# Performance work log

Hardware: AMD Instinct MI355X
Metric: run time of the kernel (lower is better)

The kernel has to match this reference:

```python
import math
import jax, jax.numpy as jnp
import numpy as np

NUM_HEADS = 8
TOP_M = 5
CLAMP_LOGIT = 2.0
LN_EPS = 1e-5


def _layernorm(x, w, b):
    m = jnp.mean(x, axis=-1, keepdims=True)
    v = jnp.mean((x - m) ** 2, axis=-1, keepdims=True)
    return (x - m) * jax.lax.rsqrt(v + LN_EPS) * w + b


def _l2norm(x, eps=1e-6):
    n = jnp.sqrt(jnp.sum(x * x, axis=-1, keepdims=True))
    return x / jnp.maximum(n, eps)


def setup_inputs() -> dict:
    key = jax.random.key(0)
    ks = jax.random.split(key, 20)
    B, H, W, Cv = 8, 64, 64, 512
    T, Ct = 77, 512
    s = 0.02
    inp = {
        'visual_features': jax.random.normal(ks[0], (B, H, W, Cv), jnp.float32),
        'text_features': jax.random.normal(ks[1], (B, T, Ct), jnp.float32),
        'norm1_w': jnp.ones((Cv,), jnp.float32),
        'norm1_b': jnp.zeros((Cv,), jnp.float32),
        'Wq': jax.random.normal(ks[2], (Cv, Cv), jnp.float32) * s,
        'bq': jnp.zeros((Cv,), jnp.float32),
        'Wk': jax.random.normal(ks[3], (Ct, Cv), jnp.float32) * s,
        'bk': jnp.zeros((Cv,), jnp.float32),
        'Wv': jax.random.normal(ks[4], (Ct, Cv), jnp.float32) * s,
        'bv': jnp.zeros((Cv,), jnp.float32),
        'Wo': jax.random.normal(ks[5], (Cv, Cv), jnp.float32) * s,
        'bo': jnp.zeros((Cv,), jnp.float32),
        'gate_w': jax.random.normal(ks[6], (Cv, 1), jnp.float32) * s,
        'gate_b': jnp.zeros((1,), jnp.float32),
        'norm2_w': jnp.ones((Cv,), jnp.float32),
        'norm2_b': jnp.zeros((Cv,), jnp.float32),
        'ffn_w1': jax.random.normal(ks[7], (Cv, 4 * Cv), jnp.float32) * s,
        'ffn_b1': jnp.zeros((4 * Cv,), jnp.float32),
        'ffn_w2': jax.random.normal(ks[8], (4 * Cv, Cv), jnp.float32) * s,
        'ffn_b2': jnp.zeros((Cv,), jnp.float32),
        'logit_scale': jnp.asarray(math.log(1.0 / 0.07), jnp.float32),
        'alpha': jnp.asarray(0.1, jnp.float32),
    }
    return inp


def reference(visual_features, text_features, norm1_w, norm1_b, Wq, bq, Wk, bk,
              Wv, bv, Wo, bo, gate_w, gate_b, norm2_w, norm2_b,
              ffn_w1, ffn_b1, ffn_w2, ffn_b2, logit_scale, alpha):
    B, H, W, Cv = visual_features.shape
    N = H * W
    Hh = NUM_HEADS
    Dh = Cv // Hh

    # Pre-LN + projections
    x = _layernorm(visual_features, norm1_w, norm1_b).reshape(B, N, Cv)
    q_full = x @ Wq + bq                       # (B,N,Cv)
    k_full = text_features @ Wk + bk           # (B,T,Cv)
    v_full = text_features @ Wv + bv           # (B,T,Cv)

    # pad mask: all-zero text tokens (B,T)
    pad_mask = jnp.sum(jnp.abs(text_features), axis=-1) <= 1e-6

    # cosine attention: normalize over full Cv before splitting heads (as in source)
    q = _l2norm(q_full).reshape(B, N, Hh, Dh)
    k = _l2norm(k_full).reshape(B, -1, Hh, Dh)
    v = v_full.reshape(B, -1, Hh, Dh)

    scale = jnp.exp(jnp.clip(logit_scale, -CLAMP_LOGIT, CLAMP_LOGIT)) / math.sqrt(Dh)
    sim = jnp.einsum('bnhd,bthd->bnht', q, k) * scale  # (B,N,Hh,T)
    sim = jnp.where(pad_mask[:, None, None, :], -jnp.inf, sim)

    # top-k sparsification along text dim (keep entries >= k-th largest)
    if TOP_M < sim.shape[-1]:
        topv = jax.lax.top_k(sim, TOP_M)[0]
        kth = topv[..., -1:]
        sim = jnp.where(sim >= kth, sim, -jnp.inf)

    attn = jax.nn.softmax(sim, axis=-1)
    aligned = jnp.einsum('bnht,bthd->bnhd', attn, v).reshape(B, N, Cv)
    aligned = aligned @ Wo + bo

    gate = jax.nn.sigmoid(x @ gate_w + gate_b)  # (B,N,1)
    y = x + alpha * gate * aligned
    y = _layernorm(y, norm2_w, norm2_b)
    h = jax.nn.gelu(y @ ffn_w1 + ffn_b1, approximate=False)
    y = y + (h @ ffn_w2 + ffn_b2)
    return y.reshape(B, H, W, Cv)
```

## Files before the change

### kernel.cpp

```cpp
#include <hip/hip_runtime.h>
#include <hip/hip_bf16.h>
#include <math.h>

constexpr int Bv = 8;
constexpr int Nv = 4096;
constexpr int Cvd = 512;
constexpr int Tt = 77;
constexpr int Dh = 64;
constexpr int MROWS = Bv * Nv;
constexpr int KTROWS = Bv * Tt;

typedef __attribute__((ext_vector_type(8))) short bf16x8;
typedef __attribute__((ext_vector_type(4))) float f32x4;

__device__ __forceinline__ float bfbits2f(short s) {
    unsigned int u = ((unsigned int)(unsigned short)s) << 16;
    return __uint_as_float(u);
}

__device__ __forceinline__ void gload16(const void* g, void* l) {
    __builtin_amdgcn_global_load_lds(
        (const __attribute__((address_space(1))) void*)g,
        (__attribute__((address_space(3))) void*)l, 16, 0, 0);
}

__device__ __forceinline__ void block_barrier() {
    asm volatile("" ::: "memory");
    __builtin_amdgcn_s_barrier();
    asm volatile("" ::: "memory");
}

__global__ __launch_bounds__(256)
void wtrans4_kernel(const float* __restrict__ Wq, const float* __restrict__ Wo,
                    const float* __restrict__ w1, const float* __restrict__ w2,
                    __hip_bfloat16* __restrict__ WqT, __hip_bfloat16* __restrict__ WoT,
                    __hip_bfloat16* __restrict__ w1T, __hip_bfloat16* __restrict__ w2T)
{
    __shared__ float tile[32][33];
    const int bid = blockIdx.x;
    const float* in;
    __hip_bfloat16* out;
    int K, N, tid;
    if (bid < 256)       { in = Wq; out = WqT; K = 512;  N = 512;  tid = bid; }
    else if (bid < 512)  { in = Wo; out = WoT; K = 512;  N = 512;  tid = bid - 256; }
    else if (bid < 1536) { in = w1; out = w1T; K = 512;  N = 2048; tid = bid - 512; }
    else                 { in = w2; out = w2T; K = 2048; N = 512;  tid = bid - 1536; }
    const int nx = N >> 5;
    const int n0 = (tid % nx) * 32, k0 = (tid / nx) * 32;
    const int tx = threadIdx.x & 31, ty = threadIdx.x >> 5;
    #pragma unroll
    for (int i = ty; i < 32; i += 8)
        tile[i][tx] = in[(size_t)(k0 + i) * N + n0 + tx];
    __syncthreads();
    #pragma unroll
    for (int i = ty; i < 32; i += 8)
        out[(size_t)(n0 + i) * K + k0 + tx] = __float2bfloat16(tile[tx][i]);
}

template<bool GATE>
__global__ __launch_bounds__(128)
void ln_kernel(const float* __restrict__ in, const float* __restrict__ w,
               const float* __restrict__ b, float* __restrict__ out,
               __hip_bfloat16* __restrict__ out_bf,
               const float* __restrict__ gate_w, const float* __restrict__ gate_b,
               float* __restrict__ gate_out)
{
    __shared__ float red[4];
    __shared__ float redg[2];
    const int row = blockIdx.x;
    const int t = threadIdx.x;
    const int wv = t >> 6;
    const float4 v = ((const float4*)(in + (size_t)row * Cvd))[t];

    float s  = v.x + v.y + v.z + v.w;
    float ss = v.x*v.x + v.y*v.y + v.z*v.z + v.w*v.w;
    #pragma unroll
    for (int o = 1; o < 64; o <<= 1) {
        s  += __shfl_xor(s,  o);
        ss += __shfl_xor(ss, o);
    }
    if ((t & 63) == 0) { red[wv*2] = s; red[wv*2+1] = ss; }
    __syncthreads();
    s  = red[0] + red[2];
    ss = red[1] + red[3];
    const float m   = s * (1.0f / 512.0f);
    const float var = ss * (1.0f / 512.0f) - m * m;
    const float rs  = 1.0f / sqrtf(var + 1e-5f);

    const float4 w4 = ((const float4*)w)[t];
    const float4 b4 = ((const float4*)b)[t];
    float4 o4;
    o4.x = (v.x - m) * rs * w4.x + b4.x;
    o4.y = (v.y - m) * rs * w4.y + b4.y;
    o4.z = (v.z - m) * rs * w4.z + b4.z;
    o4.w = (v.w - m) * rs * w4.w + b4.w;
    ((float4*)(out + (size_t)row * Cvd))[t] = o4;

    __hip_bfloat162 h0, h1;
    h0.x = __float2bfloat16(o4.x); h0.y = __float2bfloat16(o4.y);
    h1.x = __float2bfloat16(o4.z); h1.y = __float2bfloat16(o4.w);
    __hip_bfloat16* obp = out_bf + (size_t)row * Cvd + 4*t;
    *(__hip_bfloat162*)(obp)     = h0;
    *(__hip_bfloat162*)(obp + 2) = h1;

    if (GATE) {
        const float4 g4 = ((const float4*)gate_w)[t];
        float g = o4.x*g4.x + o4.y*g4.y + o4.z*g4.z + o4.w*g4.w;
        #pragma unroll
        for (int o = 1; o < 64; o <<= 1) g += __shfl_xor(g, o);
        if ((t & 63) == 0) redg[wv] = g;
        __syncthreads();
        if (t == 0) {
            const float gt = redg[0] + redg[1] + gate_b[0];
            gate_out[row] = 1.0f / (1.0f + expf(-gt));
        }
    }
}

__global__ __launch_bounds__(64)
void rownorm_bf_kernel(const __hip_bfloat16* __restrict__ src, float* __restrict__ inv)
{
    const int row = blockIdx.x;
    const int l = threadIdx.x;
    const bf16x8 v = ((const bf16x8*)(src + (size_t)row * Cvd))[l];
    float ss = 0.0f;
    #pragma unroll
    for (int j = 0; j < 8; j++) {
        const float f = bfbits2f(v[j]);
        ss += f * f;
    }
    #pragma unroll
    for (int o = 1; o < 64; o <<= 1) ss += __shfl_xor(ss, o);
    if (l == 0) inv[row] = 1.0f / fmaxf(sqrtf(ss), 1e-6f);
}

__global__ __launch_bounds__(64)
void knorm_mask_kernel(const float* __restrict__ kf, const float* __restrict__ text,
                       float* __restrict__ kinv, float* __restrict__ msk)
{
    const int row = blockIdx.x;
    const int l = threadIdx.x;
    const float4* rp = (const float4*)(kf + (size_t)row * Cvd);
    const float4* tp = (const float4*)(text + (size_t)row * Cvd);
    const float4 a = rp[l], c = rp[l + 64];
    const float4 ta = tp[l], tc = tp[l + 64];
    float ss = a.x*a.x + a.y*a.y + a.z*a.z + a.w*a.w
             + c.x*c.x + c.y*c.y + c.z*c.z + c.w*c.w;
    float sa = fabsf(ta.x)+fabsf(ta.y)+fabsf(ta.z)+fabsf(ta.w)
             + fabsf(tc.x)+fabsf(tc.y)+fabsf(tc.z)+fabsf(tc.w);
    #pragma unroll
    for (int o = 1; o < 64; o <<= 1) {
        ss += __shfl_xor(ss, o);
        sa += __shfl_xor(sa, o);
    }
    if (l == 0) {
        kinv[row] = 1.0f / fmaxf(sqrtf(ss), 1e-6f);
        msk[row]  = (sa <= 1e-6f) ? 1.0f : 0.0f;
    }
}

__global__ __launch_bounds__(256)
void gemm32kv_kernel(const float* __restrict__ A,
                     const float* __restrict__ Wk, const float* __restrict__ bk,
                     float* __restrict__ Ck,
                     const float* __restrict__ Wv, const float* __restrict__ bv,
                     float* __restrict__ Cv2,
                     int M, int K)
{
    __shared__ float As[16][64 + 4];
    __shared__ float Bs[16][64 + 4];

    const float* W    = blockIdx.z ? Wv  : Wk;
    const float* bias = blockIdx.z ? bv  : bk;
    float*       C    = blockIdx.z ? Cv2 : Ck;

    const int t = threadIdx.x;
    const int tx = t & 15, ty = t >> 4;
    const int row0 = blockIdx.y * 64;
    const int col0 = blockIdx.x * 64;

    const int arow = t >> 2;
    const int ak   = (t & 3) << 2;
    const int brow = t >> 4;
    const int bcol = (t & 15) << 2;

    float acc[4][4] = {};

    for (int kt = 0; kt < K; kt += 16) {
        float4 a4 = make_float4(0.f, 0.f, 0.f, 0.f);
        const int gr = row0 + arow;
        if (gr < M) a4 = *(const float4*)(A + (size_t)gr * 512 + kt + ak);
        As[ak + 0][arow] = a4.x;
        As[ak + 1][arow] = a4.y;
        As[ak + 2][arow] = a4.z;
        As[ak + 3][arow] = a4.w;
        const float4 b4 = *(const float4*)(W + (size_t)(kt + brow) * 512 + col0 + bcol);
        *(float4*)&Bs[brow][bcol] = b4;
        __syncthreads();
        #pragma unroll
        for (int k = 0; k < 16; k++) {
            const float4 av = *(const float4*)&As[k][ty << 2];
            const float4 bv4 = *(const float4*)&Bs[k][tx << 2];
            acc[0][0] += av.x * bv4.x; acc[0][1] += av.x * bv4.y;
            acc[0][2] += av.x * bv4.z; acc[0][3] += av.x * bv4.w;
            acc[1][0] += av.y * bv4.x; acc[1][1] += av.y * bv4.y;
            acc[1][2] += av.y * bv4.z; acc[1][3] += av.y * bv4.w;
            acc[2][0] += av.z * bv4.x; acc[2][1] += av.z * bv4.y;
            acc[2][2] += av.z * bv4.z; acc[2][3] += av.z * bv4.w;
            acc[3][0] += av.w * bv4.x; acc[3][1] += av.w * bv4.y;
            acc[3][2] += av.w * bv4.z; acc[3][3] += av.w * bv4.w;
        }
        __syncthreads();
    }

    #pragma unroll
    for (int i = 0; i < 4; i++) {
        const int r = row0 + (ty << 2) + i;
        if (r >= M) continue;
        #pragma unroll
        for (int j = 0; j < 4; j++) {
            const int c = col0 + (tx << 2) + j;
            C[(size_t)r * 512 + c] = acc[i][j] + bias[c];
        }
    }
}

enum { EPI_NONE = 0, EPI_WO = 1, EPI_GELU = 2, EPI_RES = 3, EPI_QBF = 4 };

template<int NT, int EPI>
__global__ __launch_bounds__(256, 3)
void bgemm_kernel(const __hip_bfloat16* __restrict__ Ah,
                  const __hip_bfloat16* __restrict__ Bth,
                  const float* __restrict__ bias,
                  void* __restrict__ Cout,
                  int M, int N,
                  const float* __restrict__ xres,
                  const float* __restrict__ gate,
                  const float* __restrict__ alpha_p,
                  const float* __restrict__ yres)
{
    constexpr int K = NT * 32;
    __shared__ short lds[3 * 8192];

    const short* A  = (const short*)Ah;
    const short* Bt = (const short*)Bth;

    const int nwg = gridDim.x;
    const int cpx = nwg >> 3;
    const int bid0 = blockIdx.x;
    const int bid = (bid0 & 7) * cpx + (bid0 >> 3);
    const int cols = N >> 7;
    const int row0 = (bid / cols) << 7;
    const int col0 = (bid % cols) << 7;

    const int t = threadIdx.x;
    const int w = t >> 6, l = t & 63;
    const int wr = w >> 1, wc = w & 1;

    const int src_kelem = (((l & 3) ^ ((l >> 3) & 3)) << 3);
    const short* pA0;
    const short* pA1;
    const short* pB0;
    const short* pB1;
    {
        const int r0 = (2*w)*16 + (l >> 2);
        const int r1 = (2*w + 1)*16 + (l >> 2);
        pA0 = A  + (size_t)(row0 + r0) * K + src_kelem;
        pA1 = A  + (size_t)(row0 + r1) * K + src_kelem;
        pB0 = Bt + (size_t)(col0 + r0) * K + src_kelem;
        pB1 = Bt + (size_t)(col0 + r1) * K + src_kelem;
    }
    short* const dA = lds + (2*w) * 512;
    short* const dB = lds + 4096 + (2*w) * 512;

    auto STAGE = [&](int kt, int bW) {
        gload16(pA0 + kt * 32, dA + bW * 8192);
        gload16(pA1 + kt * 32, dA + bW * 8192 + 512);
        gload16(pB0 + kt * 32, dB + bW * 8192);
        gload16(pB1 + kt * 32, dB + bW * 8192 + 512);
    };

    const int axk = (((l >> 4) << 4) ^ (((l >> 1) & 3) << 4));
    const char* const bA = (const char*)lds + (wr*64 + (l & 15))*64 + axk;
    const char* const bB = (const char*)lds + 8192 + (wc*64 + (l & 15))*64 + axk;

    bf16x8 a[4], b[4];
    f32x4 acc[4][4] = {};

    auto RD = [&](int bR) {
        #pragma unroll
        for (int i = 0; i < 4; i++)
            a[i] = *(const bf16x8*)(bA + bR*16384 + i*1024);
        #pragma unroll
        for (int i = 0; i < 4; i++)
            b[i] = *(const bf16x8*)(bB + bR*16384 + i*1024);
    };
    auto MF = [&]() {
        __builtin_amdgcn_s_setprio(1);
        #pragma unroll
        for (int i = 0; i < 4; i++)
            #pragma unroll
            for (int ni = 0; ni < 4; ni++)
                acc[i][ni] = __builtin_amdgcn_mfma_f32_16x16x32_bf16(
                    a[i], b[ni], acc[i][ni], 0, 0, 0);
        __builtin_amdgcn_s_setprio(0);
    };

    STAGE(0, 0); STAGE(1, 1);
    asm volatile("s_waitcnt vmcnt(4)" ::: "memory");
    block_barrier();

    #pragma unroll
    for (int kt = 0; kt < NT; ++kt) {
        const int bR = kt % 3;
        RD(bR);
        if (kt + 2 < NT) {
            STAGE(kt + 2, (kt + 2) % 3);
            asm volatile("s_waitcnt vmcnt(4)" ::: "memory");
        } else if (kt + 1 < NT) {
            asm volatile("s_waitcnt vmcnt(0)" ::: "memory");
        }
        block_barrier();
        MF();
        if (kt + 1 < NT) block_barrier();
    }

    const float alpha = (EPI == EPI_WO) ? alpha_p[0] : 0.0f;
    #pragma unroll
    for (int mi = 0; mi < 4; mi++) {
        const int rbase = row0 + wr*64 + mi*16 + ((l >> 4) << 2);
        #pragma unroll
        for (int ni = 0; ni < 4; ni++) {
            const int c = col0 + wc*64 + ni*16 + (l & 15);
            const float bc = bias[c];
            #pragma unroll
            for (int r = 0; r < 4; r++) {
                const int rr = rbase + r;
                const size_t idx = (size_t)rr * N + c;
                float val = acc[mi][ni][r] + bc;
                if (EPI == EPI_GELU) {
                    const float u = 1.5957691216f * val
                                  + 0.0713548163f * val * val * val;
                    val = val / (1.0f + __expf(-u));
                    ((__hip_bfloat16*)Cout)[idx] = __float2bfloat16(val);
                } else if (EPI == EPI_QBF) {
                    ((__hip_bfloat16*)Cout)[idx] = __float2bfloat16(val);
                } else if (EPI == EPI_WO) {
                    ((float*)Cout)[idx] = xres[idx] + alpha * gate[rr] * val;
                } else if (EPI == EPI_RES) {
                    ((float*)Cout)[idx] = yres[idx] + val;
                } else {
                    ((float*)Cout)[idx] = val;
                }
            }
        }
    }
}

__global__ __launch_bounds__(256)
void attn_kernel(const __hip_bfloat16* __restrict__ qf, const float* __restrict__ kf,
                 const float* __restrict__ vf, const float* __restrict__ qinv,
                 const float* __restrict__ kinv, const float* __restrict__ msk,
                 const float* __restrict__ logit_scale,
                 __hip_bfloat16* __restrict__ out)
{
    __shared__ float k_lds[Tt][Dh + 4];
    __shared__ float v_lds[Tt][Dh + 4];
    __shared__ float kinv_s[Tt];
    __shared__ float msk_s[Tt];

    const int gid = blockIdx.x;
    const int b = gid >> 7;
    const int h = (gid >> 4) & 7;
    const int ntile = gid & 15;
    const int t = threadIdx.x;

    for (int idx = t; idx < Tt * Dh; idx += 256) {
        const int tt = idx >> 6, dd = idx & 63;
        k_lds[tt][dd] = kf[(size_t)(b * Tt + tt) * Cvd + h * Dh + dd];
        v_lds[tt][dd] = vf[(size_t)(b * Tt + tt) * Cvd + h * Dh + dd];
    }
    if (t < Tt) {
        kinv_s[t] = kinv[b * Tt + t];
        msk_s[t]  = msk[b * Tt + t];
    }
    __syncthreads();

    float ls = logit_scale[0];
    ls = fminf(fmaxf(ls, -2.0f), 2.0f);
    const float scale = expf(ls) * 0.125f;

    const int wave = t >> 6, lane = t & 63;
    const int row = b * Nv + ntile * 256 + wave * 64 + lane;

    float q[Dh];
    const bf16x8* qp = (const bf16x8*)(qf + (size_t)row * Cvd + h * Dh);
    #pragma unroll
    for (int i = 0; i < 8; i++) {
        const bf16x8 x = qp[i];
        #pragma unroll
        for (int j = 0; j < 8; j++) q[8*i + j] = bfbits2f(x[j]);
    }
    const float qsc = qinv[row] * scale;

    float v0 = -INFINITY, v1 = -INFINITY, v2 = -INFINITY, v3 = -INFINITY, v4 = -INFINITY;
    int   i0 = 0, i1 = 0, i2 = 0, i3 = 0, i4 = 0;

    for (int tt = 0; tt < Tt; tt++) {
        float s = 0.0f;
        const float4* kp = (const float4*)&k_lds[tt][0];
        #pragma unroll
        for (int i = 0; i < 16; i++) {
            const float4 kx = kp[i];
            s += q[4*i] * kx.x + q[4*i+1] * kx.y + q[4*i+2] * kx.z + q[4*i+3] * kx.w;
        }
        s = s * qsc * kinv_s[tt];
        if (msk_s[tt] != 0.0f) s = -INFINITY;

        const bool c0 = s > v0, c1 = s > v1, c2 = s > v2, c3 = s > v3, c4 = s > v4;
        const float nv0 = c0 ? s : v0;               const int ni0 = c0 ? tt : i0;
        const float nv1 = c1 ? (c0 ? v0 : s) : v1;   const int ni1 = c1 ? (c0 ? i0 : tt) : i1;
        const float nv2 = c2 ? (c1 ? v1 : s) : v2;   const int ni2 = c2 ? (c1 ? i1 : tt) : i2;
        const float nv3 = c3 ? (c2 ? v2 : s) : v3;   const int ni3 = c3 ? (c2 ? i2 : tt) : i3;
        const float nv4 = c4 ? (c3 ? v3 : s) : v4;   const int ni4 = c4 ? (c3 ? i3 : tt) : i4;
        v0 = nv0; v1 = nv1; v2 = nv2; v3 = nv3; v4 = nv4;
        i0 = ni0; i1 = ni1; i2 = ni2; i3 = ni3; i4 = ni4;
    }

    const float m = v0;
    const float e0 = __expf(v0 - m), e1 = __expf(v1 - m), e2 = __expf(v2 - m),
                e3 = __expf(v3 - m), e4 = __expf(v4 - m);
    const float inv = 1.0f / (e0 + e1 + e2 + e3 + e4);
    const float w0 = e0 * inv, w1 = e1 * inv, w2 = e2 * inv, w3 = e3 * inv, w4 = e4 * inv;

    __hip_bfloat16* op = out + (size_t)row * Cvd + h * Dh;
    #pragma unroll
    for (int i = 0; i < 16; i++) {
        const float4 p0 = *(const float4*)&v_lds[i0][4*i];
        const float4 p1 = *(const float4*)&v_lds[i1][4*i];
        const float4 p2 = *(const float4*)&v_lds[i2][4*i];
        const float4 p3 = *(const float4*)&v_lds[i3][4*i];
        const float4 p4 = *(const float4*)&v_lds[i4][4*i];
        float4 a;
        a.x = w0*p0.x + w1*p1.x + w2*p2.x + w3*p3.x + w4*p4.x;
        a.y = w0*p0.y + w1*p1.y + w2*p2.y + w3*p3.y + w4*p4.y;
        a.z = w0*p0.z + w1*p1.z + w2*p2.z + w3*p3.z + w4*p4.z;
        a.w = w0*p0.w + w1*p1.w + w2*p2.w + w3*p3.w + w4*p4.w;
        __hip_bfloat162 h0, h1;
        h0.x = __float2bfloat16(a.x); h0.y = __float2bfloat16(a.y);
        h1.x = __float2bfloat16(a.z); h1.y = __float2bfloat16(a.w);
        *(__hip_bfloat162*)&op[4*i]     = h0;
        *(__hip_bfloat162*)&op[4*i + 2] = h1;
    }
}

extern "C" void kernel_launch(void* const* d_in, const int* in_sizes, int n_in,
                              void* d_out, int out_size, void* d_ws, size_t ws_size,
                              hipStream_t stream)
{
    const float* visual = (const float*)d_in[0];
    const float* text   = (const float*)d_in[1];
    const float* n1w = (const float*)d_in[2];
    const float* n1b = (const float*)d_in[3];
    const float* Wq  = (const float*)d_in[4];
    const float* bq  = (const float*)d_in[5];
    const float* Wk  = (const float*)d_in[6];
    const float* bk  = (const float*)d_in[7];
    const float* Wv  = (const float*)d_in[8];
    const float* bv  = (const float*)d_in[9];
    const float* Wo  = (const float*)d_in[10];
    const float* bo  = (const float*)d_in[11];
    const float* gw  = (const float*)d_in[12];
    const float* gb  = (const float*)d_in[13];
    const float* n2w = (const float*)d_in[14];
    const float* n2b = (const float*)d_in[15];
    const float* w1  = (const float*)d_in[16];
    const float* b1  = (const float*)d_in[17];
    const float* w2  = (const float*)d_in[18];
    const float* b2  = (const float*)d_in[19];
    const float* lsc = (const float*)d_in[20];
    const float* alp = (const float*)d_in[21];

    float* out = (float*)d_out;
    char*  w8  = (char*)d_ws;

    __hip_bfloat16* qbf    = (__hip_bfloat16*)(w8 + 0);
    float*          ypre   = (float*)(w8 + 67108864);
    __hip_bfloat16* hidden = (__hip_bfloat16*)(w8 + 0);
    __hip_bfloat16* xbf    = (__hip_bfloat16*)(w8 + 134217728);
    float*          kf     = (float*)(w8 + 167772160);
    float*          vf     = (float*)(w8 + 169033728);
    float*          qinv   = (float*)(w8 + 170295296);
    float*          kinv   = (float*)(w8 + 170426368);
    float*          mskp   = (float*)(w8 + 170428832);
    float*          gate   = (float*)(w8 + 170431296);
    __hip_bfloat16* WqT    = (__hip_bfloat16*)(w8 + 170562368);
    __hip_bfloat16* WoT    = (__hip_bfloat16*)(w8 + 171086656);
    __hip_bfloat16* w1T    = (__hip_bfloat16*)(w8 + 171610944);
    __hip_bfloat16* w2T    = (__hip_bfloat16*)(w8 + 173708096);

    wtrans4_kernel<<<dim3(2560), dim3(256), 0, stream>>>(
        Wq, Wo, w1, w2, WqT, WoT, w1T, w2T);

    ln_kernel<true><<<dim3(MROWS), dim3(128), 0, stream>>>(
        visual, n1w, n1b, out, xbf, gw, gb, gate);

    bgemm_kernel<16, EPI_QBF><<<dim3(1024), dim3(256), 0, stream>>>(
        xbf, WqT, bq, qbf, MROWS, 512, nullptr, nullptr, nullptr, nullptr);

    gemm32kv_kernel<<<dim3(8, 10, 2), dim3(256), 0, stream>>>(
        text, Wk, bk, kf, Wv, bv, vf, KTROWS, 512);

    rownorm_bf_kernel<<<dim3(MROWS), dim3(64), 0, stream>>>(qbf, qinv);
    knorm_mask_kernel<<<dim3(KTROWS), dim3(64), 0, stream>>>(kf, text, kinv, mskp);

    attn_kernel<<<dim3(1024), dim3(256), 0, stream>>>(
        qbf, kf, vf, qinv, kinv, mskp, lsc, xbf);

    bgemm_kernel<16, EPI_WO><<<dim3(1024), dim3(256), 0, stream>>>(
        xbf, WoT, bo, ypre, MROWS, 512, out, gate, alp, nullptr);

    ln_kernel<false><<<dim3(MROWS), dim3(128), 0, stream>>>(
        ypre, n2w, n2b, out, xbf, nullptr, nullptr, nullptr);

    bgemm_kernel<16, EPI_GELU><<<dim3(4096), dim3(256), 0, stream>>>(
        xbf, w1T, b1, hidden, MROWS, 2048, nullptr, nullptr, nullptr, nullptr);

    bgemm_kernel<64, EPI_RES><<<dim3(1024), dim3(256), 0, stream>>>(
        hidden, w2T, b2, out, MROWS, 512, nullptr, nullptr, nullptr, out);
}
```

Measured before the change: 455.7 us.

## Load GEMM B operand directly to registers instead of staging through LDS

```diff
diff --git a/kernel.cpp b/kernel.cpp
--- a/kernel.cpp
+++ b/kernel.cpp
@@ -240,7 +240,7 @@
                   const float* __restrict__ yres)
 {
     constexpr int K = NT * 32;
-    __shared__ short lds[3 * 8192];
+    __shared__ short lds[3 * 4096];
 
     const short* A  = (const short*)Ah;
     const short* Bt = (const short*)Bth;
@@ -260,68 +260,67 @@
     const int src_kelem = (((l & 3) ^ ((l >> 3) & 3)) << 3);
     const short* pA0;
     const short* pA1;
-    const short* pB0;
-    const short* pB1;
     {
         const int r0 = (2*w)*16 + (l >> 2);
         const int r1 = (2*w + 1)*16 + (l >> 2);
-        pA0 = A  + (size_t)(row0 + r0) * K + src_kelem;
-        pA1 = A  + (size_t)(row0 + r1) * K + src_kelem;
-        pB0 = Bt + (size_t)(col0 + r0) * K + src_kelem;
-        pB1 = Bt + (size_t)(col0 + r1) * K + src_kelem;
+        pA0 = A + (size_t)(row0 + r0) * K + src_kelem;
+        pA1 = A + (size_t)(row0 + r1) * K + src_kelem;
     }
     short* const dA = lds + (2*w) * 512;
-    short* const dB = lds + 4096 + (2*w) * 512;
-
-    auto STAGE = [&](int kt, int bW) {
-        gload16(pA0 + kt * 32, dA + bW * 8192);
-        gload16(pA1 + kt * 32, dA + bW * 8192 + 512);
-        gload16(pB0 + kt * 32, dB + bW * 8192);
-        gload16(pB1 + kt * 32, dB + bW * 8192 + 512);
+
+    auto STAGE_A = [&](int kt, int bW) {
+        gload16(pA0 + kt * 32, dA + bW * 4096);
+        gload16(pA1 + kt * 32, dA + bW * 4096 + 512);
+    };
+
+    const short* pBf0 = Bt + (size_t)(col0 + wc*64 +  0 + (l & 15)) * K + ((l >> 4) << 3);
+    const short* pBf1 = Bt + (size_t)(col0 + wc*64 + 16 + (l & 15)) * K + ((l >> 4) << 3);
+    const short* pBf2 = Bt + (size_t)(col0 + wc*64 + 32 + (l & 15)) * K + ((l >> 4) << 3);
+    const short* pBf3 = Bt + (size_t)(col0 + wc*64 + 48 + (l & 15)) * K + ((l >> 4) << 3);
+
+    bf16x8 breg[3][4];
+    auto LOADB = [&](int kt, int rb) {
+        breg[rb][0] = *(const bf16x8*)(pBf0 + kt * 32);
+        breg[rb][1] = *(const bf16x8*)(pBf1 + kt * 32);
+        breg[rb][2] = *(const bf16x8*)(pBf2 + kt * 32);
+        breg[rb][3] = *(const bf16x8*)(pBf3 + kt * 32);
     };
 
     const int axk = (((l >> 4) << 4) ^ (((l >> 1) & 3) << 4));
     const char* const bA = (const char*)lds + (wr*64 + (l & 15))*64 + axk;
-    const char* const bB = (const char*)lds + 8192 + (wc*64 + (l & 15))*64 + axk;
-
-    bf16x8 a[4], b[4];
+
+    bf16x8 a[4];
     f32x4 acc[4][4] = {};
 
-    auto RD = [&](int bR) {
+    auto RD_A = [&](int bR) {
         #pragma unroll
         for (int i = 0; i < 4; i++)
-            a[i] = *(const bf16x8*)(bA + bR*16384 + i*1024);
-        #pragma unroll
-        for (int i = 0; i < 4; i++)
-            b[i] = *(const bf16x8*)(bB + bR*16384 + i*1024);
+            a[i] = *(const bf16x8*)(bA + bR*8192 + i*1024);
     };
-    auto MF = [&]() {
-        __builtin_amdgcn_s_setprio(1);
+
+    STAGE_A(0, 0); LOADB(0, 0);
+    STAGE_A(1, 1); LOADB(1, 1);
+    asm volatile("s_waitcnt vmcnt(6)" ::: "memory");
+    block_barrier();
+
+    #pragma unroll
+    for (int kt = 0; kt < NT; ++kt) {
+        const int bR = kt % 3;
+        RD_A(bR);
+        if (kt + 2 < NT) {
+            STAGE_A(kt + 2, (kt + 2) % 3);
+            LOADB(kt + 2, (kt + 2) % 3);
+            asm volatile("s_waitcnt vmcnt(6)" ::: "memory");
+        } else if (kt + 1 < NT) {
+            asm volatile("s_waitcnt vmcnt(0)" ::: "memory");
+        }
+        block_barrier();
         #pragma unroll
         for (int i = 0; i < 4; i++)
             #pragma unroll
             for (int ni = 0; ni < 4; ni++)
                 acc[i][ni] = __builtin_amdgcn_mfma_f32_16x16x32_bf16(
-                    a[i], b[ni], acc[i][ni], 0, 0, 0);
-        __builtin_amdgcn_s_setprio(0);
-    };
-
-    STAGE(0, 0); STAGE(1, 1);
-    asm volatile("s_waitcnt vmcnt(4)" ::: "memory");
-    block_barrier();
-
-    #pragma unroll
-    for (int kt = 0; kt < NT; ++kt) {
-        const int bR = kt % 3;
-        RD(bR);
-        if (kt + 2 < NT) {
-            STAGE(kt + 2, (kt + 2) % 3);
-            asm volatile("s_waitcnt vmcnt(4)" ::: "memory");
-        } else if (kt + 1 < NT) {
-            asm volatile("s_waitcnt vmcnt(0)" ::: "memory");
-        }
-        block_barrier();
-        MF();
+                    a[i], breg[bR][ni], acc[i][ni], 0, 0, 0);
         if (kt + 1 < NT) block_barrier();
     }
 
```

Result: slower. 574.5 us (+26.1%).

## Compute attention scores with bf16 MFMA using pre-normalized bf16 keys

Applied to the files above, without the earlier changes.

```diff
diff --git a/kernel.cpp b/kernel.cpp
--- a/kernel.cpp
+++ b/kernel.cpp
@@ -16,6 +16,10 @@
 __device__ __forceinline__ float bfbits2f(short s) {
     unsigned int u = ((unsigned int)(unsigned short)s) << 16;
     return __uint_as_float(u);
+}
+__device__ __forceinline__ short f2bfbits(float f) {
+    __hip_bfloat16 h = __float2bfloat16(f);
+    return *reinterpret_cast<short*>(&h);
 }
 
 __device__ __forceinline__ void gload16(const void* g, void* l) {
@@ -136,7 +140,7 @@
 
 __global__ __launch_bounds__(64)
 void knorm_mask_kernel(const float* __restrict__ kf, const float* __restrict__ text,
-                       float* __restrict__ kinv, float* __restrict__ msk)
+                       float* __restrict__ msk, __hip_bfloat16* __restrict__ kbf)
 {
     const int row = blockIdx.x;
     const int l = threadIdx.x;
@@ -153,10 +157,19 @@
         ss += __shfl_xor(ss, o);
         sa += __shfl_xor(sa, o);
     }
-    if (l == 0) {
-        kinv[row] = 1.0f / fmaxf(sqrtf(ss), 1e-6f);
-        msk[row]  = (sa <= 1e-6f) ? 1.0f : 0.0f;
-    }
+    const float ki = 1.0f / fmaxf(sqrtf(ss), 1e-6f);
+    if (l == 0) msk[row] = (sa <= 1e-6f) ? 1.0f : 0.0f;
+
+    __hip_bfloat16* kp = kbf + (size_t)row * Cvd;
+    __hip_bfloat162 p;
+    p.x = __float2bfloat16(a.x * ki); p.y = __float2bfloat16(a.y * ki);
+    *(__hip_bfloat162*)(kp + l*4)     = p;
+    p.x = __float2bfloat16(a.z * ki); p.y = __float2bfloat16(a.w * ki);
+    *(__hip_bfloat162*)(kp + l*4 + 2) = p;
+    p.x = __float2bfloat16(c.x * ki); p.y = __float2bfloat16(c.y * ki);
+    *(__hip_bfloat162*)(kp + (l+64)*4)     = p;
+    p.x = __float2bfloat16(c.z * ki); p.y = __float2bfloat16(c.w * ki);
+    *(__hip_bfloat162*)(kp + (l+64)*4 + 2) = p;
 }
 
 __global__ __launch_bounds__(256)
@@ -358,99 +371,130 @@
 }
 
 __global__ __launch_bounds__(256)
-void attn_kernel(const __hip_bfloat16* __restrict__ qf, const float* __restrict__ kf,
-                 const float* __restrict__ vf, const float* __restrict__ qinv,
-                 const float* __restrict__ kinv, const float* __restrict__ msk,
+void attn_kernel(const __hip_bfloat16* __restrict__ qf,
+                 const __hip_bfloat16* __restrict__ kbf,
+                 const float* __restrict__ vf,
+                 const float* __restrict__ qinv,
+                 const float* __restrict__ msk,
                  const float* __restrict__ logit_scale,
                  __hip_bfloat16* __restrict__ out)
 {
-    __shared__ float k_lds[Tt][Dh + 4];
-    __shared__ float v_lds[Tt][Dh + 4];
-    __shared__ float kinv_s[Tt];
-    __shared__ float msk_s[Tt];
+    __shared__ short kb[80 * 72];
+    __shared__ float v_lds[Tt][68];
+    __shared__ float qinv_s[256];
+    __shared__ float bias_s[80];
 
     const int gid = blockIdx.x;
     const int b = gid >> 7;
     const int h = (gid >> 4) & 7;
     const int ntile = gid & 15;
     const int t = threadIdx.x;
-
+    const int row0 = b * Nv + ntile * 256;
+
+    #pragma unroll
+    for (int it = 0; it < 3; ++it) {
+        const int ch = t + it * 256;
+        if (ch < 616) {
+            const int row = ch >> 3, part = ch & 7;
+            *(bf16x8*)&kb[row * 72 + part * 8] =
+                *(const bf16x8*)(kbf + (size_t)(b * Tt + row) * Cvd + h * Dh + part * 8);
+        }
+    }
+    if (t < 27) {
+        const bf16x8 z = {0,0,0,0,0,0,0,0};
+        *(bf16x8*)&kb[77 * 72 + t * 8] = z;
+    }
     for (int idx = t; idx < Tt * Dh; idx += 256) {
         const int tt = idx >> 6, dd = idx & 63;
-        k_lds[tt][dd] = kf[(size_t)(b * Tt + tt) * Cvd + h * Dh + dd];
         v_lds[tt][dd] = vf[(size_t)(b * Tt + tt) * Cvd + h * Dh + dd];
     }
-    if (t < Tt) {
-        kinv_s[t] = kinv[b * Tt + t];
-        msk_s[t]  = msk[b * Tt + t];
-    }
+    qinv_s[t] = qinv[row0 + t];
+    if (t < 80) bias_s[t] = (t < 77 && msk[b * Tt + t] == 0.0f) ? 0.0f : -1e30f;
     __syncthreads();
 
     float ls = logit_scale[0];
     ls = fminf(fmaxf(ls, -2.0f), 2.0f);
-    const float scale = expf(ls) * 0.125f;
-
-    const int wave = t >> 6, lane = t & 63;
-    const int row = b * Nv + ntile * 256 + wave * 64 + lane;
-
-    float q[Dh];
-    const bf16x8* qp = (const bf16x8*)(qf + (size_t)row * Cvd + h * Dh);
-    #pragma unroll
-    for (int i = 0; i < 8; i++) {
-        const bf16x8 x = qp[i];
-        #pragma unroll
-        for (int j = 0; j < 8; j++) q[8*i + j] = bfbits2f(x[j]);
-    }
-    const float qsc = qinv[row] * scale;
-
-    float v0 = -INFINITY, v1 = -INFINITY, v2 = -INFINITY, v3 = -INFINITY, v4 = -INFINITY;
-    int   i0 = 0, i1 = 0, i2 = 0, i3 = 0, i4 = 0;
-
-    for (int tt = 0; tt < Tt; tt++) {
-        float s = 0.0f;
-        const float4* kp = (const float4*)&k_lds[tt][0];
-        #pragma unroll
-        for (int i = 0; i < 16; i++) {
-            const float4 kx = kp[i];
-            s += q[4*i] * kx.x + q[4*i+1] * kx.y + q[4*i+2] * kx.z + q[4*i+3] * kx.w;
-        }
-        s = s * qsc * kinv_s[tt];
-        if (msk_s[tt] != 0.0f) s = -INFINITY;
-
-        const bool c0 = s > v0, c1 = s > v1, c2 = s > v2, c3 = s > v3, c4 = s > v4;
-        const float nv0 = c0 ? s : v0;               const int ni0 = c0 ? tt : i0;
-        const float nv1 = c1 ? (c0 ? v0 : s) : v1;   const int ni1 = c1 ? (c0 ? i0 : tt) : i1;
-        const float nv2 = c2 ? (c1 ? v1 : s) : v2;   const int ni2 = c2 ? (c1 ? i1 : tt) : i2;
-        const float nv3 = c3 ? (c2 ? v2 : s) : v3;   const int ni3 = c3 ? (c2 ? i2 : tt) : i3;
-        const float nv4 = c4 ? (c3 ? v3 : s) : v4;   const int ni4 = c4 ? (c3 ? i3 : tt) : i4;
-        v0 = nv0; v1 = nv1; v2 = nv2; v3 = nv3; v4 = nv4;
-        i0 = ni0; i1 = ni1; i2 = ni2; i3 = ni3; i4 = ni4;
-    }
-
-    const float m = v0;
-    const float e0 = __expf(v0 - m), e1 = __expf(v1 - m), e2 = __expf(v2 - m),
-                e3 = __expf(v3 - m), e4 = __expf(v4 - m);
-    const float inv = 1.0f / (e0 + e1 + e2 + e3 + e4);
-    const float w0 = e0 * inv, w1 = e1 * inv, w2 = e2 * inv, w3 = e3 * inv, w4 = e4 * inv;
-
-    __hip_bfloat16* op = out + (size_t)row * Cvd + h * Dh;
-    #pragma unroll
-    for (int i = 0; i < 16; i++) {
-        const float4 p0 = *(const float4*)&v_lds[i0][4*i];
-        const float4 p1 = *(const float4*)&v_lds[i1][4*i];
-        const float4 p2 = *(const float4*)&v_lds[i2][4*i];
-        const float4 p3 = *(const float4*)&v_lds[i3][4*i];
-        const float4 p4 = *(const float4*)&v_lds[i4][4*i];
-        float4 a;
-        a.x = w0*p0.x + w1*p1.x + w2*p2.x + w3*p3.x + w4*p4.x;
-        a.y = w0*p0.y + w1*p1.y + w2*p2.y + w3*p3.y + w4*p4.y;
-        a.z = w0*p0.z + w1*p1.z + w2*p2.z + w3*p3.z + w4*p4.z;
-        a.w = w0*p0.w + w1*p1.w + w2*p2.w + w3*p3.w + w4*p4.w;
-        __hip_bfloat162 h0, h1;
-        h0.x = __float2bfloat16(a.x); h0.y = __float2bfloat16(a.y);
-        h1.x = __float2bfloat16(a.z); h1.y = __float2bfloat16(a.w);
-        *(__hip_bfloat162*)&op[4*i]     = h0;
-        *(__hip_bfloat162*)&op[4*i + 2] = h1;
+    const float scale = __expf(ls) * 0.125f;
+
+    const int w = t >> 6, l = t & 63;
+    const int c = l & 15, g = l >> 4;
+
+    bf16x8 qfrag[8];
+    #pragma unroll
+    for (int rt = 0; rt < 4; ++rt)
+        #pragma unroll
+        for (int kk = 0; kk < 2; ++kk)
+            qfrag[rt*2 + kk] = *(const bf16x8*)(qf +
+                (size_t)(row0 + w*64 + rt*16 + c) * Cvd + h * Dh + kk*32 + g*8);
+
+    #pragma unroll
+    for (int rt = 0; rt < 4; ++rt) {
+        const int lrow = w*64 + rt*16 + c;
+        const float qsc = qinv_s[lrow] * scale;
+
+        float v0=-INFINITY,v1=-INFINITY,v2=-INFINITY,v3=-INFINITY,v4=-INFINITY;
+        int   i0=0,i1=0,i2=0,i3=0,i4=0;
+        auto INS = [&](float s, int idx) {
+            const bool c0=s>v0, c1=s>v1, c2=s>v2, c3=s>v3, c4=s>v4;
+            const float nv0=c0?s:v0;              const int ni0=c0?idx:i0;
+            const float nv1=c1?(c0?v0:s):v1;      const int ni1=c1?(c0?i0:idx):i1;
+            const float nv2=c2?(c1?v1:s):v2;      const int ni2=c2?(c1?i1:idx):i2;
+            const float nv3=c3?(c2?v2:s):v3;      const int ni3=c3?(c2?i2:idx):i3;
+            const float nv4=c4?(c3?v3:s):v4;      const int ni4=c4?(c3?i3:idx):i4;
+            v0=nv0;v1=nv1;v2=nv2;v3=nv3;v4=nv4;
+            i0=ni0;i1=ni1;i2=ni2;i3=ni3;i4=ni4;
+        };
+
+        #pragma unroll
+        for (int kt = 0; kt < 5; ++kt) {
+            f32x4 acc = {0.f, 0.f, 0.f, 0.f};
+            const bf16x8 ka0 = *(const bf16x8*)&kb[(kt*16 + c) * 72 + g*8];
+            const bf16x8 ka1 = *(const bf16x8*)&kb[(kt*16 + c) * 72 + 32 + g*8];
+            acc = __builtin_amdgcn_mfma_f32_16x16x32_bf16(ka0, qfrag[rt*2+0], acc, 0, 0, 0);
+            acc = __builtin_amdgcn_mfma_f32_16x16x32_bf16(ka1, qfrag[rt*2+1], acc, 0, 0, 0);
+            #pragma unroll
+            for (int r = 0; r < 4; ++r) {
+                const int key = kt*16 + g*4 + r;
+                INS(acc[r] * qsc + bias_s[key], key);
+            }
+        }
+
+        #pragma unroll
+        for (int st = 16; st <= 32; st <<= 1) {
+            const float m0=__shfl_xor(v0,st), m1=__shfl_xor(v1,st),
+                        m2=__shfl_xor(v2,st), m3=__shfl_xor(v3,st),
+                        m4=__shfl_xor(v4,st);
+            const int   j0=__shfl_xor(i0,st), j1=__shfl_xor(i1,st),
+                        j2=__shfl_xor(i2,st), j3=__shfl_xor(i3,st),
+                        j4=__shfl_xor(i4,st);
+            INS(m0,j0); INS(m1,j1); INS(m2,j2); INS(m3,j3); INS(m4,j4);
+        }
+
+        const float e1=__expf(v1-v0), e2=__expf(v2-v0),
+                    e3=__expf(v3-v0), e4=__expf(v4-v0);
+        const float inv = 1.0f / (1.0f + e1 + e2 + e3 + e4);
+        const float w0=inv, w1=e1*inv, w2=e2*inv, w3=e3*inv, w4=e4*inv;
+
+        float o[16];
+        #pragma unroll
+        for (int d4 = 0; d4 < 4; ++d4) {
+            const int dd = g*16 + d4*4;
+            const float4 p0 = *(const float4*)&v_lds[i0][dd];
+            const float4 p1 = *(const float4*)&v_lds[i1][dd];
+            const float4 p2 = *(const float4*)&v_lds[i2][dd];
+            const float4 p3 = *(const float4*)&v_lds[i3][dd];
+            const float4 p4 = *(const float4*)&v_lds[i4][dd];
+            o[d4*4+0] = w0*p0.x + w1*p1.x + w2*p2.x + w3*p3.x + w4*p4.x;
+            o[d4*4+1] = w0*p0.y + w1*p1.y + w2*p2.y + w3*p3.y + w4*p4.y;
+            o[d4*4+2] = w0*p0.z + w1*p1.z + w2*p2.z + w3*p3.z + w4*p4.z;
+            o[d4*4+3] = w0*p0.w + w1*p1.w + w2*p2.w + w3*p3.w + w4*p4.w;
+        }
+        __hip_bfloat16* op = out + (size_t)(row0 + lrow) * Cvd + h * Dh + g*16;
+        bf16x8 s0, s1;
+        #pragma unroll
+        for (int j = 0; j < 8; ++j) { s0[j] = f2bfbits(o[j]); s1[j] = f2bfbits(o[8+j]); }
+        *(bf16x8*)op       = s0;
+        *(bf16x8*)(op + 8) = s1;
     }
 }
 
@@ -491,13 +535,13 @@
     float*          kf     = (float*)(w8 + 167772160);
     float*          vf     = (float*)(w8 + 169033728);
     float*          qinv   = (float*)(w8 + 170295296);
-    float*          kinv   = (float*)(w8 + 170426368);
     float*          mskp   = (float*)(w8 + 170428832);
     float*          gate   = (float*)(w8 + 170431296);
     __hip_bfloat16* WqT    = (__hip_bfloat16*)(w8 + 170562368);
     __hip_bfloat16* WoT    = (__hip_bfloat16*)(w8 + 171086656);
     __hip_bfloat16* w1T    = (__hip_bfloat16*)(w8 + 171610944);
     __hip_bfloat16* w2T    = (__hip_bfloat16*)(w8 + 173708096);
+    __hip_bfloat16* kbfg   = (__hip_bfloat16*)(w8 + 175805248);
 
     wtrans4_kernel<<<dim3(2560), dim3(256), 0, stream>>>(
         Wq, Wo, w1, w2, WqT, WoT, w1T, w2T);
@@ -512,10 +556,10 @@
         text, Wk, bk, kf, Wv, bv, vf, KTROWS, 512);
 
     rownorm_bf_kernel<<<dim3(MROWS), dim3(64), 0, stream>>>(qbf, qinv);
-    knorm_mask_kernel<<<dim3(KTROWS), dim3(64), 0, stream>>>(kf, text, kinv, mskp);
+    knorm_mask_kernel<<<dim3(KTROWS), dim3(64), 0, stream>>>(kf, text, mskp, kbfg);
 
     attn_kernel<<<dim3(1024), dim3(256), 0, stream>>>(
-        qbf, kf, vf, qinv, kinv, mskp, lsc, xbf);
+        qbf, kbfg, vf, qinv, mskp, lsc, xbf);
 
     bgemm_kernel<16, EPI_WO><<<dim3(1024), dim3(256), 0, stream>>>(
         xbf, WoT, bo, ypre, MROWS, 512, out, gate, alp, nullptr);
```

Measured after the change: 408.0 us. 10.5% less time.
